# Kernel optimization log

Hardware: AMD Instinct MI355X
Metric: run time of the kernel (lower is better)

## Reference

```python
import jax, jax.numpy as jnp
import numpy as np

N0, N1 = 30000, 20000
N = N0 + N1
E = 400000
H0, H1, H2 = 4, 4, 1
DH = 64            # num_hidden
NC = 16            # num_classes
IN = 128           # per-type input feature dim
SLOPE = 0.2        # leaky relu negative slope


def setup_inputs() -> dict:
    key = jax.random.key(0)
    ks = iter(jax.random.split(key, 48))
    rn = lambda shape, s=0.05: jax.random.normal(next(ks), shape, jnp.float32) * s
    ri = lambda shape: jax.random.randint(next(ks), shape, 0, N, jnp.int32)
    inp = {
        'features0': rn((N0, IN), 1.0),
        'features1': rn((N1, IN), 1.0),
        'fc_w0': rn((IN, DH)), 'fc_b0': jnp.zeros((DH,), jnp.float32),
        'fc_w1': rn((IN, DH)), 'fc_b1': jnp.zeros((DH,), jnp.float32),
        'mix_w': jnp.zeros((2, 3, 2), jnp.float32),  # (n_types, num_layers+1, n_graphs)
        # GATConv params stacked over the 2 relation graphs
        'W0': rn((2, DH, H0 * DH)), 'al0': rn((2, H0, DH), 0.1), 'ar0': rn((2, H0, DH), 0.1), 'b0': jnp.zeros((2, H0 * DH), jnp.float32),
        'W1': rn((2, H0 * DH, H1 * DH)), 'al1': rn((2, H1, DH), 0.1), 'ar1': rn((2, H1, DH), 0.1), 'b1': jnp.zeros((2, H1 * DH), jnp.float32),
        'W2': rn((2, H1 * DH, H2 * NC)), 'al2': rn((2, H2, NC), 0.1), 'ar2': rn((2, H2, NC), 0.1), 'b2': jnp.zeros((2, H2 * NC), jnp.float32),
        'res2': rn((2, H1 * DH, H2 * NC)),  # res_fc for last layer (in != out*heads)
        'src0': ri((E,)), 'dst0': ri((E,)),
        'src1': ri((E,)), 'dst1': ri((E,)),
    }
    return inp


def gat_conv(h, src, dst, W, al, ar, b, H, D, res_mode, res_w, act):
    # h: (N, in)  ->  (N, H, D)
    feat = (h @ W).reshape(N, H, D)
    el = jnp.sum(feat * al, axis=-1)   # (N, H)
    er = jnp.sum(feat * ar, axis=-1)   # (N, H)
    e = jax.nn.leaky_relu(el[src] + er[dst], SLOPE)  # (E, H)
    # edge softmax over incoming edges of each dst node
    m = jax.ops.segment_max(e, dst, num_segments=N)
    ex = jnp.exp(e - m[dst])
    den = jax.ops.segment_sum(ex, dst, num_segments=N)
    alpha = ex / den[dst]                              # (E, H)
    out = jax.ops.segment_sum(feat[src] * alpha[..., None], dst, num_segments=N)
    if res_mode == 'id':
        out = out + h.reshape(N, H, D)
    elif res_mode == 'fc':
        out = out + (h @ res_w).reshape(N, H, D)
    out = out + b.reshape(1, H, D)
    return jax.nn.elu(out) if act else out


def _forward(features0, features1, fc_w0, fc_b0, fc_w1, fc_b1, mix_w,
             W0, al0, ar0, b0, W1, al1, ar1, b1, W2, al2, ar2, b2, res2,
             src0, dst0, src1, dst1):
    nt = jnp.concatenate([jnp.zeros(N0, jnp.int32), jnp.ones(N1, jnp.int32)])
    w = jax.nn.softmax(mix_w, axis=2)  # (types, layers+1, graphs)
    h = jnp.concatenate([features0 @ fc_w0 + fc_b0, features1 @ fc_w1 + fc_b1], axis=0)
    srcs, dsts = (src0, src1), (dst0, dst1)
    layers = [
        (W0, al0, ar0, b0, H0, DH, None, True),
        (W1, al1, ar1, b1, H1, DH, 'id', True),
    ]
    for l, (W, al, ar, b, H, D, rm, act) in enumerate(layers):
        acc = 0.
        for i in range(2):
            o = gat_conv(h, srcs[i], dsts[i], W[i], al[i], ar[i], b[i], H, D, rm, None, act)
            acc = acc + o.reshape(N, H * D) * w[nt, l, i][:, None]
        h = acc
    logits = 0.
    for i in range(2):
        o = gat_conv(h, srcs[i], dsts[i], W2[i], al2[i], ar2[i], b2[i], H2, NC, 'fc', res2[i], False)
        logits = logits + o.mean(axis=1) * w[nt, 2, i][:, None]
    return logits


def reference(features0, features1, fc_w0, fc_b0, fc_w1, fc_b1, mix_w,
              W0, al0, ar0, b0, W1, al1, ar1, b1, W2, al2, ar2, b2, res2,
              src0, dst0, src1, dst1):
    return _forward(features0, features1, fc_w0, fc_b0, fc_w1, fc_b1, mix_w,
                    W0, al0, ar0, b0, W1, al1, ar1, b1, W2, al2, ar2, b2, res2,
                    src0, dst0, src1, dst1)
```

## Files before the change

kernel.cpp:

```cpp
#include <hip/hip_runtime.h>
#include <hip/hip_bf16.h>

#define NN   50000
#define NN0  30000
#define EE   400000
#define NB_SCAN ((NN + 1023) / 1024)
#define NRT   3125
#define NGRP  ((NRT + 3) / 4)
#define NT0   1875

typedef unsigned short u16;
typedef unsigned int   u32;

typedef __attribute__((ext_vector_type(8))) __bf16 bf16x8;
typedef __attribute__((ext_vector_type(4))) float  f32x4;

__device__ __forceinline__ float bf2f(u16 u){ return __uint_as_float(((u32)u)<<16); }
__device__ __forceinline__ float lo16(u32 u){ return __uint_as_float(u<<16); }
__device__ __forceinline__ float hi16(u32 u){ return __uint_as_float(u & 0xffff0000u); }
__device__ __forceinline__ u16 f2bf(float f){
  u32 x = __float_as_uint(f);
  x += 0x7fffu + ((x>>16)&1u);
  return (u16)(x>>16);
}
__device__ __forceinline__ float elu_f(float x){ return x>0.f ? x : __expf(x)-1.f; }
__device__ __forceinline__ float lrelu(float x){ return x>0.f ? x : 0.2f*x; }
__device__ __forceinline__ bf16x8 ld_frag(const u16* p){
  uint4 v = *(const uint4*)p;
  return __builtin_bit_cast(bf16x8, v);
}
__device__ __forceinline__ bf16x8 cvt8(const float* p){
  float4 u = ((const float4*)p)[0];
  float4 v = ((const float4*)p)[1];
  u32 w0 = (u32)f2bf(u.x) | ((u32)f2bf(u.y)<<16);
  u32 w1 = (u32)f2bf(u.z) | ((u32)f2bf(u.w)<<16);
  u32 w2 = (u32)f2bf(v.x) | ((u32)f2bf(v.y)<<16);
  u32 w3 = (u32)f2bf(v.z) | ((u32)f2bf(v.w)<<16);
  uint4 r{w0,w1,w2,w3};
  return __builtin_bit_cast(bf16x8, r);
}

__global__ __launch_bounds__(256) void k_prep(
    const float* __restrict__ mix_w, float* __restrict__ wsoft,
    const float* __restrict__ W0, u16* __restrict__ W0p,
    const float* __restrict__ W1, u16* __restrict__ W1p,
    const float* __restrict__ W2, const float* __restrict__ res2, u16* __restrict__ W2p,
    const float* __restrict__ fcw0, const float* __restrict__ fcw1, u16* __restrict__ Fp,
    const float* __restrict__ al0, const float* __restrict__ ar0, u16* __restrict__ Vp)
{
  int t = blockIdx.x*256 + threadIdx.x;
  if (t < 6){
    float a0 = mix_w[t*2+0], a1 = mix_w[t*2+1];
    float mx = fmaxf(a0,a1);
    float e0 = __expf(a0-mx), e1 = __expf(a1-mx);
    wsoft[t*2+0] = e0/(e0+e1); wsoft[t*2+1] = e1/(e0+e1);
  }
  if (t < 4096){
    int gg = t>>11, fi = t&2047;
    int lane = fi&63, kb = (fi>>6)&1, ct = fi>>7;
    int q = lane>>4, c = lane&15;
    const float* src = W0 + (size_t)gg*16384;
    u16* o = W0p + (size_t)gg*16384 + (size_t)fi*8;
    #pragma unroll
    for (int j=0;j<8;j++) o[j] = f2bf(src[(size_t)(kb*32+q*8+j)*256 + ct*16 + c]);
  } else if (t < 20480){
    int u = t - 4096;
    int gg = u>>13, fi = u&8191;
    int lane = fi&63, kb = (fi>>6)&7, ct = fi>>9;
    int q = lane>>4, c = lane&15;
    const float* src = W1 + (size_t)gg*65536;
    u16* o = W1p + (size_t)gg*65536 + (size_t)fi*8;
    #pragma unroll
    for (int j=0;j<8;j++) o[j] = f2bf(src[(size_t)(kb*32+q*8+j)*256 + ct*16 + c]);
  } else if (t < 22528){
    int fi = t - 20480;
    int lane = fi&63, kb = (fi>>6)&7, ct = fi>>9;
    int q = lane>>4, c = lane&15;
    int cl = ct*16 + c;
    int i = cl>>5, which = (cl>>4)&1;
    const float* src = which ? res2 : W2;
    u16* o = W2p + (size_t)fi*8;
    #pragma unroll
    for (int j=0;j<8;j++) o[j] = f2bf(src[(size_t)i*4096 + (size_t)(kb*32+q*8+j)*16 + (cl&15)]);
  } else if (t < 24576){
    int u = t - 22528;
    int tt = u>>10, fi = u&1023;
    int lane = fi&63, kb = (fi>>6)&3, ct = fi>>8;
    int q = lane>>4, c = lane&15;
    const float* src = tt ? fcw1 : fcw0;
    u16* o = Fp + (size_t)tt*8192 + (size_t)fi*8;
    #pragma unroll
    for (int j=0;j<8;j++) o[j] = f2bf(src[(size_t)(kb*32+q*8+j)*64 + ct*16 + c]);
  } else if (t < 25600){
    int u = t - 24576;
    int fi = u>>3, j = u&7;
    int lane = fi&63, kb = fi>>6;
    int q = lane>>4, c = lane&15;
    int k = kb*32 + q*8 + j;
    int which = c>>3, g=(c>>2)&1, h=c&3;
    const float* sel = (which ? ar0 : al0) + (size_t)(g*4+h)*64;
    const float* Wrow = W0 + (size_t)g*16384 + (size_t)k*256 + h*64;
    float s=0.f;
    #pragma unroll 8
    for (int d=0;d<64;d++) s = fmaf(Wrow[d], sel[d], s);
    Vp[(size_t)fi*8 + j] = f2bf(s);
  }
}

__global__ void k_count2(const int* __restrict__ d0, const int* __restrict__ d1,
                         int* __restrict__ cnt2){
  int t = blockIdx.x*256 + threadIdx.x;
  int g = blockIdx.y;
  if (t < EE) atomicAdd(&cnt2[g*NN + (g ? d1[t] : d0[t])], 1);
}

__global__ __launch_bounds__(1024) void k_scan1(const int* __restrict__ cnt2,
                                                int* __restrict__ row2, int* __restrict__ bsum){
  __shared__ int wsum[16];
  int g = blockIdx.y;
  int lane = threadIdx.x & 63, wid = threadIdx.x >> 6;
  int i = blockIdx.x*1024 + threadIdx.x;
  int v = (i < NN) ? cnt2[g*NN + i] : 0;
  int x = v;
  #pragma unroll
  for (int off = 1; off < 64; off <<= 1){
    int y = __shfl_up(x, off, 64);
    if (lane >= off) x += y;
  }
  if (lane == 63) wsum[wid] = x;
  __syncthreads();
  if (wid == 0 && lane < 16){
    int s = wsum[lane];
    #pragma unroll
    for (int off = 1; off < 16; off <<= 1){
      int y = __shfl_up(s, off, 16);
      if (lane >= off) s += y;
    }
    wsum[lane] = s;
  }
  __syncthreads();
  int incl = x + (wid ? wsum[wid-1] : 0);
  if (i < NN) row2[(size_t)g*(NN+1) + i] = incl - v;
  if (threadIdx.x == 1023) bsum[g*NB_SCAN + blockIdx.x] = incl;
}

__global__ __launch_bounds__(128) void k_scan2(const int* __restrict__ bsum, int* __restrict__ boff){
  int g = threadIdx.x >> 6, lane = threadIdx.x & 63;
  int v = (lane < NB_SCAN) ? bsum[g*NB_SCAN + lane] : 0;
  int x = v;
  #pragma unroll
  for (int off = 1; off < 64; off <<= 1){
    int y = __shfl_up(x, off, 64);
    if (lane >= off) x += y;
  }
  if (lane < NB_SCAN) boff[g*NB_SCAN + lane] = x - v;
}

__global__ __launch_bounds__(1024) void k_scan3(int* __restrict__ row2, const int* __restrict__ boff){
  int g = blockIdx.y;
  int i = blockIdx.x*1024 + threadIdx.x;
  if (i < NN) row2[(size_t)g*(NN+1) + i] += boff[g*NB_SCAN + blockIdx.x];
  if (blockIdx.x == 0 && threadIdx.x == 0) row2[(size_t)g*(NN+1) + NN] = EE;
}

__global__ void k_scatter2(const int* __restrict__ s0, const int* __restrict__ d0,
                           const int* __restrict__ s1, const int* __restrict__ d1,
                           const int* __restrict__ row2, int* __restrict__ fill2,
                           u16* __restrict__ col2, u16* __restrict__ dstOf){
  int t = blockIdx.x*256 + threadIdx.x;
  int g = blockIdx.y;
  if (t >= EE) return;
  int d = g ? d1[t] : d0[t];
  int s = g ? s1[t] : s0[t];
  int pos = atomicAdd(&fill2[g*NN + d], 1);
  size_t slot = (size_t)g*EE + row2[(size_t)g*(NN+1) + d] + pos;
  col2[slot]  = (u16)s;
  dstOf[slot] = (u16)d;
}

__global__ void k_alpha4(const u16* __restrict__ col2, const u16* __restrict__ dstOf,
                         const float* __restrict__ el, const float* __restrict__ er,
                         size_t elStride, float* __restrict__ xbuf){
  int t = blockIdx.x*256 + threadIdx.x;
  int g = blockIdx.y;
  if (t >= EE) return;
  size_t slot = (size_t)g*EE + t;
  int s = col2[slot], d = dstOf[slot];
  const float* elg = el + (size_t)g*elStride;
  const float* erg = er + (size_t)g*elStride;
  float4 e4 = ((const float4*)elg)[s];
  float4 r4 = ((const float4*)erg)[d];
  float4 x;
  x.x = __expf(lrelu(e4.x + r4.x));
  x.y = __expf(lrelu(e4.y + r4.y));
  x.z = __expf(lrelu(e4.z + r4.z));
  x.w = __expf(lrelu(e4.w + r4.w));
  ((float4*)xbuf)[slot] = x;
}

__global__ void k_alpha1(const u16* __restrict__ col2, const u16* __restrict__ dstOf,
                         const float* __restrict__ el2, const float* __restrict__ er2,
                         float* __restrict__ xb2){
  int t = blockIdx.x*256 + threadIdx.x;
  int g = blockIdx.y;
  if (t >= EE) return;
  size_t slot = (size_t)g*EE + t;
  int s = col2[slot], d = dstOf[slot];
  xb2[slot] = __expf(lrelu(el2[(size_t)g*NN + s] + er2[(size_t)g*NN + d]));
}

__global__ __launch_bounds__(256) void k_inproj_m(
    const float* __restrict__ f0, const float* __restrict__ f1,
    const u16* __restrict__ Fp, const float* __restrict__ fb0, const float* __restrict__ fb1,
    u16* __restrict__ h0)
{
  int wv = threadIdx.x>>6, ln = threadIdx.x&63;
  int ti = blockIdx.x*4 + wv;
  if (ti >= NRT) return;
  int q = ln>>4, c = ln&15;
  int type = (ti < NT0) ? 0 : 1;
  const float* F = type ? f1 : f0;
  int rbase = type ? (ti*16 - NN0) : ti*16;
  const u16* Bg = Fp + (size_t)type*8192;
  const float* bb = type ? fb1 : fb0;
  f32x4 acc[4] = {};
  const float* Ap = F + (size_t)(rbase + c)*128;
  #pragma unroll
  for (int kb=0; kb<4; kb++){
    bf16x8 a = cvt8(Ap + kb*32 + q*8);
    #pragma unroll
    for (int ct=0; ct<4; ct++){
      bf16x8 b = ld_frag(Bg + ((size_t)(ct*4+kb)*64 + ln)*8);
      acc[ct] = __builtin_amdgcn_mfma_f32_16x16x32_bf16(a, b, acc[ct], 0,0,0);
    }
  }
  #pragma unroll
  for (int ct=0; ct<4; ct++){
    float bv = bb[ct*16+c];
    #pragma unroll
    for (int j=0;j<4;j++){
      int row = ti*16 + q*4 + j;
      h0[(size_t)row*64 + ct*16 + c] = f2bf(acc[ct][j] + bv);
    }
  }
}

__global__ __launch_bounds__(256) void k_eler0(
    const u16* __restrict__ h0, const u16* __restrict__ Vp,
    float* __restrict__ elA, float* __restrict__ erA)
{
  int wv = threadIdx.x>>6, ln = threadIdx.x&63;
  int ti = blockIdx.x*4 + wv;
  if (ti >= NRT) return;
  int q = ln>>4, c = ln&15;
  f32x4 acc = {};
  const u16* Ap = h0 + (size_t)(ti*16 + c)*64 + q*8;
  #pragma unroll
  for (int kb=0; kb<2; kb++){
    bf16x8 a = ld_frag(Ap + kb*32);
    bf16x8 b = ld_frag(Vp + ((size_t)(kb*64 + ln))*8);
    acc = __builtin_amdgcn_mfma_f32_16x16x32_bf16(a, b, acc, 0,0,0);
  }
  int which = c>>3, g = (c>>2)&1, h = c&3;
  float* dst = (which ? erA : elA) + (size_t)g*NN*4;
  #pragma unroll
  for (int j=0;j<4;j++){
    int row = ti*16 + q*4 + j;
    dst[row*4 + h] = acc[j];
  }
}

__global__ __launch_bounds__(256) void k_agg0(
    const int* __restrict__ row2, const u16* __restrict__ col2,
    const float* __restrict__ xbuf, const u16* __restrict__ h0,
    u16* __restrict__ aggB, size_t aggStride)
{
  int wv = threadIdx.x>>6, ln = threadIdx.x&63;
  int n = blockIdx.x*4 + wv;
  #pragma unroll
  for (int g=0; g<2; g++){
    const int* rw = row2 + (size_t)g*(NN+1);
    const u16* cl = col2 + (size_t)g*EE;
    const float4* xb = (const float4*)xbuf + (size_t)g*EE;
    int beg = rw[n], end = rw[n+1];
    float d0=0.f,d1=0.f,d2=0.f,d3=0.f;
    float a0=0.f,a1=0.f,a2=0.f,a3=0.f;
    int k = beg;
    for (; k+2<=end; k+=2){
      int s0 = cl[k], s1 = cl[k+1];
      float4 x0 = xb[k], x1 = xb[k+1];
      float v0 = bf2f(h0[(size_t)s0*64 + ln]);
      float v1 = bf2f(h0[(size_t)s1*64 + ln]);
      d0 += x0.x+x1.x; d1 += x0.y+x1.y; d2 += x0.z+x1.z; d3 += x0.w+x1.w;
      a0 += x0.x*v0 + x1.x*v1; a1 += x0.y*v0 + x1.y*v1;
      a2 += x0.z*v0 + x1.z*v1; a3 += x0.w*v0 + x1.w*v1;
    }
    for (; k<end; k++){
      int s = cl[k];
      float4 x = xb[k];
      float v = bf2f(h0[(size_t)s*64 + ln]);
      d0+=x.x; d1+=x.y; d2+=x.z; d3+=x.w;
      a0+=x.x*v; a1+=x.y*v; a2+=x.z*v; a3+=x.w*v;
    }
    bool has = (end > beg);
    a0 = has ? a0/d0 : 0.f; a1 = has ? a1/d1 : 0.f;
    a2 = has ? a2/d2 : 0.f; a3 = has ? a3/d3 : 0.f;
    u16* og = aggB + (size_t)g*aggStride + (size_t)n*256 + ln;
    og[0]   = f2bf(a0); og[64]  = f2bf(a1);
    og[128] = f2bf(a2); og[192] = f2bf(a3);
  }
}

__global__ __launch_bounds__(256) void k_head0(
    const u16* __restrict__ aggB, size_t aggStride,
    const u16* __restrict__ W0p, const float* __restrict__ b0,
    const float* __restrict__ wsoft, u16* __restrict__ h1)
{
  int wv = threadIdx.x>>6, ln = threadIdx.x&63;
  int ti = blockIdx.x*4 + wv;
  if (ti >= NRT) return;
  int q = ln>>4, c = ln&15;
  int type = (ti < NT0) ? 0 : 1;
  float wg0 = wsoft[type*6 + 0];
  float wg1 = wsoft[type*6 + 1];
  for (int h=0; h<4; h++){
    f32x4 acc[2][4] = {};
    #pragma unroll
    for (int g=0; g<2; g++){
      const u16* Ap = aggB + (size_t)g*aggStride + (size_t)(ti*16 + c)*256 + h*64 + q*8;
      const u16* Bg = W0p + (size_t)g*16384;
      #pragma unroll
      for (int kb=0; kb<2; kb++){
        bf16x8 a = ld_frag(Ap + kb*32);
        #pragma unroll
        for (int ct=0; ct<4; ct++){
          int ctg = h*4 + ct;
          bf16x8 b = ld_frag(Bg + ((size_t)(ctg*2 + kb)*64 + ln)*8);
          acc[g][ct] = __builtin_amdgcn_mfma_f32_16x16x32_bf16(a, b, acc[g][ct], 0,0,0);
        }
      }
    }
    #pragma unroll
    for (int ct=0; ct<4; ct++){
      int colg = h*64 + ct*16 + c;
      float bb0 = b0[colg], bb1 = b0[256 + colg];
      #pragma unroll
      for (int j=0;j<4;j++){
        int row = ti*16 + q*4 + j;
        float o = wg0*elu_f(acc[0][ct][j] + bb0) + wg1*elu_f(acc[1][ct][j] + bb1);
        h1[(size_t)row*256 + colg] = f2bf(o);
      }
    }
  }
}

template<int K>
__global__ __launch_bounds__(256) void k_gemm4(
    const u16* __restrict__ A,
    const u16* __restrict__ Bp, size_t bpStride,
    const float* __restrict__ al, const float* __restrict__ ar, int alStride,
    u16* __restrict__ feat, size_t featStride,
    float* __restrict__ el, float* __restrict__ er, size_t elStride)
{
  constexpr int KB = K/32;
  int wv = threadIdx.x>>6, ln = threadIdx.x&63;
  int bid = blockIdx.x;
  int g = bid / NGRP, grp = bid % NGRP;
  int split = wv, q = ln>>4, c = ln&15;
  const u16* Bpg = Bp + (size_t)g*bpStride;
  const float* alg = al + (size_t)g*alStride;
  const float* arg = ar + (size_t)g*alStride;
  u16* featg = feat + (size_t)g*featStride;
  float* elg = el + (size_t)g*elStride;
  float* erg = er + (size_t)g*elStride;

  f32x4 acc[4][4] = {};
  int  tbase = grp*4;
  bool valid[4];
  const u16* Ap[4];
  #pragma unroll
  for (int rt=0; rt<4; rt++){
    int ti = tbase + rt;
    valid[rt] = (ti < NRT);
    if (!valid[rt]) ti = NRT-1;
    Ap[rt] = A + (size_t)(ti*16 + c)*K + q*8;
  }
  const u16* Bbase = Bpg + ((size_t)(split*4)*KB*64 + ln)*8;

  #pragma unroll 2
  for (int kb=0; kb<KB; kb++){
    bf16x8 b[4], a[4];
    #pragma unroll
    for (int ct=0; ct<4; ct++) b[ct] = ld_frag(Bbase + (size_t)(ct*KB + kb)*64*8);
    #pragma unroll
    for (int rt=0; rt<4; rt++) a[rt] = ld_frag(Ap[rt] + kb*32);
    #pragma unroll
    for (int rt=0; rt<4; rt++)
      #pragma unroll
      for (int ct=0; ct<4; ct++)
        acc[rt][ct] = __builtin_amdgcn_mfma_f32_16x16x32_bf16(a[rt], b[ct], acc[rt][ct], 0,0,0);
  }

  float alv[4], arv[4];
  #pragma unroll
  for (int ct=0;ct<4;ct++){
    int cg = (split*4+ct)*16 + c;
    alv[ct] = alg[cg]; arv[ct] = arg[cg];
  }
  #pragma unroll
  for (int rt=0; rt<4; rt++){
    if (!valid[rt]) continue;
    int row0 = (tbase+rt)*16;
    #pragma unroll
    for (int j=0;j<4;j++){
      float ep=0.f, rp=0.f;
      #pragma unroll
      for (int ct=0;ct<4;ct++){ ep += acc[rt][ct][j]*alv[ct]; rp += acc[rt][ct][j]*arv[ct]; }
      #pragma unroll
      for (int off=8; off; off>>=1){ ep += __shfl_xor(ep,off,16); rp += __shfl_xor(rp,off,16); }
      int row = row0 + q*4 + j;
      if (c==0){ elg[row*4+split]=ep; erg[row*4+split]=rp; }
      #pragma unroll
      for (int ct=0;ct<4;ct++)
        featg[(size_t)row*256 + (split*4+ct)*16 + c] = f2bf(acc[rt][ct][j]);
    }
  }
}

template<int RES>
__global__ __launch_bounds__(256) void k_aggNF(
    const int* __restrict__ row2, const u16* __restrict__ col2,
    const float* __restrict__ xbuf,
    const u16* __restrict__ feat, size_t featStride,
    const u16* __restrict__ hres, const float* __restrict__ bias,
    const float* __restrict__ wsoft, int l,
    u16* __restrict__ hout)
{
  int wv = threadIdx.x>>6, ln = threadIdx.x&63;
  int n = blockIdx.x*4 + wv;
  int h = ln>>4;
  int type = (n<NN0)?0:1;
  float rx=0.f, ry=0.f, rz=0.f, rw_=0.f;
  if (RES){
    uint2 r = ((const uint2*)hres)[(size_t)n*64 + ln];
    rx=lo16(r.x); ry=hi16(r.x); rz=lo16(r.y); rw_=hi16(r.y);
  }
  float o0=0.f,o1=0.f,o2=0.f,o3=0.f;
  #pragma unroll
  for (int g=0; g<2; g++){
    const int* rw = row2 + (size_t)g*(NN+1);
    const u16* cl = col2 + (size_t)g*EE;
    const float* xb = xbuf + (size_t)g*EE*4;
    const uint2* fp = (const uint2*)(feat + (size_t)g*featStride);
    int beg = rw[n], end = rw[n+1];
    float den = 0.f;
    float a0=0.f,a1=0.f,a2=0.f,a3=0.f;
    int k = beg;
    for (; k+4<=end; k+=4){
      int s0=cl[k], s1=cl[k+1], s2=cl[k+2], s3=cl[k+3];
      float x0 = xb[(size_t)k*4 + h];
      float x1 = xb[(size_t)(k+1)*4 + h];
      float x2 = xb[(size_t)(k+2)*4 + h];
      float x3 = xb[(size_t)(k+3)*4 + h];
      uint2 f0 = fp[(size_t)s0*64 + ln];
      uint2 f1 = fp[(size_t)s1*64 + ln];
      uint2 f2 = fp[(size_t)s2*64 + ln];
      uint2 f3 = fp[(size_t)s3*64 + ln];
      den += (x0+x1) + (x2+x3);
      a0 += x0*lo16(f0.x) + x1*lo16(f1.x) + x2*lo16(f2.x) + x3*lo16(f3.x);
      a1 += x0*hi16(f0.x) + x1*hi16(f1.x) + x2*hi16(f2.x) + x3*hi16(f3.x);
      a2 += x0*lo16(f0.y) + x1*lo16(f1.y) + x2*lo16(f2.y) + x3*lo16(f3.y);
      a3 += x0*hi16(f0.y) + x1*hi16(f1.y) + x2*hi16(f2.y) + x3*hi16(f3.y);
    }
    for (; k<end; k++){
      int s = cl[k];
      float x = xb[(size_t)k*4 + h];
      uint2 f = fp[(size_t)s*64 + ln];
      den += x;
      a0 += x*lo16(f.x); a1 += x*hi16(f.x); a2 += x*lo16(f.y); a3 += x*hi16(f.y);
    }
    float inv = (end>beg) ? 1.0f/den : 0.f;
    float4 bv = ((const float4*)(bias + g*256))[ln];
    a0 = a0*inv + bv.x; a1 = a1*inv + bv.y; a2 = a2*inv + bv.z; a3 = a3*inv + bv.w;
    if (RES){ a0 += rx; a1 += ry; a2 += rz; a3 += rw_; }
    float w = wsoft[type*6 + l*2 + g];
    o0 += w*elu_f(a0); o1 += w*elu_f(a1); o2 += w*elu_f(a2); o3 += w*elu_f(a3);
  }
  uint2 o;
  o.x = (u32)f2bf(o0) | ((u32)f2bf(o1)<<16);
  o.y = (u32)f2bf(o2) | ((u32)f2bf(o3)<<16);
  ((uint2*)hout)[(size_t)n*64 + ln] = o;
}

__global__ __launch_bounds__(256) void k_gemm2(
    const u16* __restrict__ A, const u16* __restrict__ Bp,
    const float* __restrict__ al2, const float* __restrict__ ar2,
    float* __restrict__ feat16, float* __restrict__ resb,
    float* __restrict__ el2, float* __restrict__ er2)
{
  int wv = threadIdx.x>>6, ln = threadIdx.x&63;
  int wt = blockIdx.x*4 + wv;
  if (wt >= NRT) return;
  int row0 = wt*16;
  int q = ln>>4, c = ln&15;
  f32x4 acc[4] = {};
  const u16* Ap = A + (size_t)(row0 + c)*256 + q*8;
  #pragma unroll
  for (int kb=0; kb<8; kb++){
    bf16x8 a = ld_frag(Ap + kb*32);
    #pragma unroll
    for (int t=0;t<4;t++){
      bf16x8 b = ld_frag(Bp + ((size_t)(t*8 + kb)*64 + ln)*8);
      acc[t] = __builtin_amdgcn_mfma_f32_16x16x32_bf16(a, b, acc[t], 0,0,0);
    }
  }
  #pragma unroll
  for (int i=0;i<2;i++){
    float alv = al2[i*16+c], arv = ar2[i*16+c];
    #pragma unroll
    for (int j=0;j<4;j++){
      float ep = acc[2*i][j]*alv, rp = acc[2*i][j]*arv;
      #pragma unroll
      for (int off=8; off; off>>=1){ ep += __shfl_xor(ep,off,16); rp += __shfl_xor(rp,off,16); }
      if (c==0){
        int row = row0 + q*4 + j;
        el2[(size_t)i*NN + row] = ep; er2[(size_t)i*NN + row] = rp;
      }
    }
    #pragma unroll
    for (int j=0;j<4;j++){
      int row = row0 + q*4 + j;
      feat16[(size_t)i*NN*16 + (size_t)row*16 + c] = acc[2*i][j];
      resb  [(size_t)i*NN*16 + (size_t)row*16 + c] = acc[2*i+1][j];
    }
  }
}

__global__ __launch_bounds__(256) void k_agg2D(
    const int* __restrict__ row2, const u16* __restrict__ col2,
    const float* __restrict__ xb2,
    const float* __restrict__ feat16, const float* __restrict__ resb,
    const float* __restrict__ b2, const float* __restrict__ wsoft,
    float* __restrict__ out)
{
  int t = threadIdx.x;
  int nl = t>>4, j = t&15;
  int n = blockIdx.x*16 + nl;
  int type = (n<NN0)?0:1;
  float o = 0.f;
  #pragma unroll
  for (int i=0;i<2;i++){
    const int* rw = row2 + (size_t)i*(NN+1);
    const u16* cl = col2 + (size_t)i*EE;
    const float* xb = xb2 + (size_t)i*EE;
    const float* f  = feat16 + (size_t)i*NN*16;
    int beg = rw[n], end = rw[n+1];
    float den = 0.f, acc = 0.f;
    int k = beg;
    for (; k+4<=end; k+=4){
      int s0=cl[k], s1=cl[k+1], s2=cl[k+2], s3=cl[k+3];
      float x0 = xb[k], x1 = xb[k+1], x2 = xb[k+2], x3 = xb[k+3];
      float v0 = f[(size_t)s0*16 + j];
      float v1 = f[(size_t)s1*16 + j];
      float v2 = f[(size_t)s2*16 + j];
      float v3 = f[(size_t)s3*16 + j];
      den += (x0+x1) + (x2+x3);
      acc += x0*v0 + x1*v1 + x2*v2 + x3*v3;
    }
    for (; k<end; k++){
      int s = cl[k];
      float x = xb[k];
      den += x;
      acc = fmaf(x, f[(size_t)s*16 + j], acc);
    }
    float inv = (end>beg) ? 1.0f/den : 0.f;
    float oi = acc*inv + b2[i*16+j] + resb[(size_t)i*NN*16 + (size_t)n*16 + j];
    o += oi * wsoft[type*6 + 4 + i];
  }
  out[(size_t)n*16 + j] = o;
}

extern "C" void kernel_launch(void* const* d_in, const int* in_sizes, int n_in,
                              void* d_out, int out_size, void* d_ws, size_t ws_size,
                              hipStream_t stream)
{
  const float* features0 = (const float*)d_in[0];
  const float* features1 = (const float*)d_in[1];
  const float* fc_w0 = (const float*)d_in[2];
  const float* fc_b0 = (const float*)d_in[3];
  const float* fc_w1 = (const float*)d_in[4];
  const float* fc_b1 = (const float*)d_in[5];
  const float* mix_w = (const float*)d_in[6];
  const float* W0  = (const float*)d_in[7];
  const float* al0 = (const float*)d_in[8];
  const float* ar0 = (const float*)d_in[9];
  const float* b0  = (const float*)d_in[10];
  const float* W1  = (const float*)d_in[11];
  const float* al1 = (const float*)d_in[12];
  const float* ar1 = (const float*)d_in[13];
  const float* b1  = (const float*)d_in[14];
  const float* W2  = (const float*)d_in[15];
  const float* al2 = (const float*)d_in[16];
  const float* ar2 = (const float*)d_in[17];
  const float* b2  = (const float*)d_in[18];
  const float* res2= (const float*)d_in[19];
  const int* src[2] = {(const int*)d_in[20], (const int*)d_in[22]};
  const int* dst[2] = {(const int*)d_in[21], (const int*)d_in[23]};
  (void)in_sizes; (void)n_in; (void)out_size; (void)ws_size;

  char* ws = (char*)d_ws;
  size_t off = 0;
  auto alloc = [&](size_t bytes)->char*{
    char* p = ws + off; off += (bytes + 255) & ~(size_t)255; return p;
  };
  float* wsoft = (float*)alloc(64*4);
  u16*   W0p   = (u16*)  alloc((size_t)2*64*256*2);
  u16*   W1p   = (u16*)  alloc((size_t)2*256*256*2);
  u16*   W2p   = (u16*)  alloc((size_t)256*64*2);
  u16*   Fp    = (u16*)  alloc((size_t)2*128*64*2);
  u16*   Vp    = (u16*)  alloc((size_t)64*16*2);
  int*   row2  = (int*)  alloc((size_t)2*(NN+1)*4);
  u16*   col2  = (u16*)  alloc((size_t)2*EE*2);
  u16*   dstOf = (u16*)  alloc((size_t)2*EE*2);
  int*   zeros = (int*)  alloc((size_t)4*NN*4);
  int*   cnt2  = zeros;
  int*   fill2 = zeros + 2*NN;
  int*   bsum  = (int*)alloc((size_t)2*NB_SCAN*4);
  int*   boff  = (int*)alloc((size_t)2*NB_SCAN*4);
  u16*   h0    = (u16*)alloc((size_t)NN*64*2);
  u16*   h1    = (u16*)alloc((size_t)NN*256*2);
  u16*   h2    = (u16*)alloc((size_t)NN*256*2);
  float* elA   = (float*)alloc((size_t)2*NN*4*4);
  float* erA   = (float*)alloc((size_t)2*NN*4*4);
  float* xbuf  = (float*)alloc((size_t)2*EE*4*4);
  size_t featStride = (size_t)NN*256;
  size_t off_D = off;
  u16* regionD = (u16*)alloc(2*featStride*2);
  u16* aggB  = regionD;
  u16* featD = regionD;
  float* feat16 = (float*)(ws + off_D);
  float* resb   = feat16 + (size_t)2*NN*16;
  float* el2    = resb   + (size_t)2*NN*16;
  float* er2    = el2    + (size_t)2*NN;

  k_prep<<<100,256,0,stream>>>(mix_w, wsoft, W0, W0p, W1, W1p, W2, res2, W2p,
                               fc_w0, fc_w1, Fp, al0, ar0, Vp);

  hipMemsetAsync(zeros, 0, (size_t)4*NN*4, stream);
  {
    dim3 gE((EE+255)/256, 2), gS(NB_SCAN, 2);
    k_count2 <<<gE,256,0,stream>>>(dst[0], dst[1], cnt2);
    k_scan1  <<<gS,1024,0,stream>>>(cnt2, row2, bsum);
    k_scan2  <<<1,128,0,stream>>>(bsum, boff);
    k_scan3  <<<gS,1024,0,stream>>>(row2, boff);
    k_scatter2<<<gE,256,0,stream>>>(src[0], dst[0], src[1], dst[1], row2, fill2, col2, dstOf);
  }

  k_inproj_m<<<NGRP,256,0,stream>>>(features0, features1, Fp, fc_b0, fc_b1, h0);
  k_eler0   <<<NGRP,256,0,stream>>>(h0, Vp, elA, erA);

  dim3 gE((EE+255)/256, 2);

  k_alpha4<<<gE,256,0,stream>>>(col2, dstOf, elA, erA, (size_t)NN*4, xbuf);
  k_agg0 <<<NN/4,256,0,stream>>>(row2, col2, xbuf, h0, aggB, featStride);
  k_head0<<<NGRP,256,0,stream>>>(aggB, featStride, W0p, b0, wsoft, h1);

  k_gemm4<256><<<2*NGRP,256,0,stream>>>(h1, W1p, (size_t)256*256, al1, ar1, 256,
                                        featD, featStride, elA, erA, (size_t)NN*4);
  k_alpha4<<<gE,256,0,stream>>>(col2, dstOf, elA, erA, (size_t)NN*4, xbuf);
  k_aggNF<1><<<NN/4,256,0,stream>>>(row2, col2, xbuf, featD, featStride,
                                    h1, b1, wsoft, 1, h2);

  k_gemm2<<<NGRP,256,0,stream>>>(h2, W2p, al2, ar2, feat16, resb, el2, er2);
  k_alpha1<<<gE,256,0,stream>>>(col2, dstOf, el2, er2, xbuf);
  k_agg2D<<<NN/16,256,0,stream>>>(row2, col2, xbuf, feat16, resb, b2, wsoft, (float*)d_out);
}
```

Measured before the change: 459.5 us.

## Compute softmax denominators per node, fuse layer-0 aggregation with head GEMM

Drops the per-edge dstOf array. Edge exp-scores are now computed per destination node over the CSR row, which also yields an inverse softmax denominator per node, so the aggregation kernels no longer sum denominators. Layer-0 aggregation and the head GEMM are fused through an LDS tile, which removes the aggB round trip through global memory. An 8-wide unrolled gather loop is added to the layer-1 aggregation. The catch is that the per-node alpha kernels use one thread per node, so degree imbalance and uncoalesced xbuf writes may hurt.

```diff
diff --git a/kernel.cpp b/kernel.cpp
--- a/kernel.cpp
+++ b/kernel.cpp
@@ -166,47 +166,67 @@
 __global__ void k_scatter2(const int* __restrict__ s0, const int* __restrict__ d0,
                            const int* __restrict__ s1, const int* __restrict__ d1,
                            const int* __restrict__ row2, int* __restrict__ fill2,
-                           u16* __restrict__ col2, u16* __restrict__ dstOf){
+                           u16* __restrict__ col2){
   int t = blockIdx.x*256 + threadIdx.x;
   int g = blockIdx.y;
   if (t >= EE) return;
   int d = g ? d1[t] : d0[t];
   int s = g ? s1[t] : s0[t];
   int pos = atomicAdd(&fill2[g*NN + d], 1);
-  size_t slot = (size_t)g*EE + row2[(size_t)g*(NN+1) + d] + pos;
-  col2[slot]  = (u16)s;
-  dstOf[slot] = (u16)d;
-}
-
-__global__ void k_alpha4(const u16* __restrict__ col2, const u16* __restrict__ dstOf,
-                         const float* __restrict__ el, const float* __restrict__ er,
-                         size_t elStride, float* __restrict__ xbuf){
-  int t = blockIdx.x*256 + threadIdx.x;
+  col2[(size_t)g*EE + row2[(size_t)g*(NN+1) + d] + pos] = (u16)s;
+}
+
+__global__ void k_alphaden4(const int* __restrict__ row2, const u16* __restrict__ col2,
+                            const float* __restrict__ el, const float* __restrict__ er,
+                            size_t elStride, float* __restrict__ xbuf,
+                            float* __restrict__ invd){
+  int n = blockIdx.x*256 + threadIdx.x;
   int g = blockIdx.y;
-  if (t >= EE) return;
-  size_t slot = (size_t)g*EE + t;
-  int s = col2[slot], d = dstOf[slot];
+  if (n >= NN) return;
+  const int* rw = row2 + (size_t)g*(NN+1);
+  const u16* cl = col2 + (size_t)g*EE;
   const float* elg = el + (size_t)g*elStride;
-  const float* erg = er + (size_t)g*elStride;
-  float4 e4 = ((const float4*)elg)[s];
-  float4 r4 = ((const float4*)erg)[d];
-  float4 x;
-  x.x = __expf(lrelu(e4.x + r4.x));
-  x.y = __expf(lrelu(e4.y + r4.y));
-  x.z = __expf(lrelu(e4.z + r4.z));
-  x.w = __expf(lrelu(e4.w + r4.w));
-  ((float4*)xbuf)[slot] = x;
-}
-
-__global__ void k_alpha1(const u16* __restrict__ col2, const u16* __restrict__ dstOf,
-                         const float* __restrict__ el2, const float* __restrict__ er2,
-                         float* __restrict__ xb2){
-  int t = blockIdx.x*256 + threadIdx.x;
+  float4 r4 = ((const float4*)(er + (size_t)g*elStride))[n];
+  float4* xb = (float4*)xbuf + (size_t)g*EE;
+  int beg = rw[n], end = rw[n+1];
+  float d0=0.f,d1=0.f,d2=0.f,d3=0.f;
+  for (int k=beg; k<end; k++){
+    int s = cl[k];
+    float4 e = ((const float4*)elg)[s];
+    float4 x;
+    x.x = __expf(lrelu(e.x + r4.x));
+    x.y = __expf(lrelu(e.y + r4.y));
+    x.z = __expf(lrelu(e.z + r4.z));
+    x.w = __expf(lrelu(e.w + r4.w));
+    xb[k] = x;
+    d0 += x.x; d1 += x.y; d2 += x.z; d3 += x.w;
+  }
+  bool has = (end > beg);
+  float4 iv;
+  iv.x = has ? 1.f/d0 : 0.f; iv.y = has ? 1.f/d1 : 0.f;
+  iv.z = has ? 1.f/d2 : 0.f; iv.w = has ? 1.f/d3 : 0.f;
+  ((float4*)invd)[(size_t)g*NN + n] = iv;
+}
+
+__global__ void k_alphaden1(const int* __restrict__ row2, const u16* __restrict__ col2,
+                            const float* __restrict__ el2, const float* __restrict__ er2,
+                            float* __restrict__ xb2, float* __restrict__ invd1){
+  int n = blockIdx.x*256 + threadIdx.x;
   int g = blockIdx.y;
-  if (t >= EE) return;
-  size_t slot = (size_t)g*EE + t;
-  int s = col2[slot], d = dstOf[slot];
-  xb2[slot] = __expf(lrelu(el2[(size_t)g*NN + s] + er2[(size_t)g*NN + d]));
+  if (n >= NN) return;
+  const int* rw = row2 + (size_t)g*(NN+1);
+  const u16* cl = col2 + (size_t)g*EE;
+  const float* elg = el2 + (size_t)g*NN;
+  float ern = er2[(size_t)g*NN + n];
+  float* xb = xb2 + (size_t)g*EE;
+  int beg = rw[n], end = rw[n+1];
+  float d = 0.f;
+  for (int k=beg; k<end; k++){
+    float x = __expf(lrelu(elg[cl[k]] + ern));
+    xb[k] = x;
+    d += x;
+  }
+  invd1[(size_t)g*NN + n] = (end>beg) ? 1.f/d : 0.f;
 }
 
 __global__ __launch_bounds__(256) void k_inproj_m(
@@ -270,86 +290,79 @@
   }
 }
 
-__global__ __launch_bounds__(256) void k_agg0(
+__global__ __launch_bounds__(256) void k_fused0(
     const int* __restrict__ row2, const u16* __restrict__ col2,
-    const float* __restrict__ xbuf, const u16* __restrict__ h0,
-    u16* __restrict__ aggB, size_t aggStride)
-{
-  int wv = threadIdx.x>>6, ln = threadIdx.x&63;
-  int n = blockIdx.x*4 + wv;
-  #pragma unroll
-  for (int g=0; g<2; g++){
-    const int* rw = row2 + (size_t)g*(NN+1);
-    const u16* cl = col2 + (size_t)g*EE;
-    const float4* xb = (const float4*)xbuf + (size_t)g*EE;
-    int beg = rw[n], end = rw[n+1];
-    float d0=0.f,d1=0.f,d2=0.f,d3=0.f;
-    float a0=0.f,a1=0.f,a2=0.f,a3=0.f;
-    int k = beg;
-    for (; k+2<=end; k+=2){
-      int s0 = cl[k], s1 = cl[k+1];
-      float4 x0 = xb[k], x1 = xb[k+1];
-      float v0 = bf2f(h0[(size_t)s0*64 + ln]);
-      float v1 = bf2f(h0[(size_t)s1*64 + ln]);
-      d0 += x0.x+x1.x; d1 += x0.y+x1.y; d2 += x0.z+x1.z; d3 += x0.w+x1.w;
-      a0 += x0.x*v0 + x1.x*v1; a1 += x0.y*v0 + x1.y*v1;
-      a2 += x0.z*v0 + x1.z*v1; a3 += x0.w*v0 + x1.w*v1;
-    }
-    for (; k<end; k++){
-      int s = cl[k];
-      float4 x = xb[k];
-      float v = bf2f(h0[(size_t)s*64 + ln]);
-      d0+=x.x; d1+=x.y; d2+=x.z; d3+=x.w;
-      a0+=x.x*v; a1+=x.y*v; a2+=x.z*v; a3+=x.w*v;
-    }
-    bool has = (end > beg);
-    a0 = has ? a0/d0 : 0.f; a1 = has ? a1/d1 : 0.f;
-    a2 = has ? a2/d2 : 0.f; a3 = has ? a3/d3 : 0.f;
-    u16* og = aggB + (size_t)g*aggStride + (size_t)n*256 + ln;
-    og[0]   = f2bf(a0); og[64]  = f2bf(a1);
-    og[128] = f2bf(a2); og[192] = f2bf(a3);
-  }
-}
-
-__global__ __launch_bounds__(256) void k_head0(
-    const u16* __restrict__ aggB, size_t aggStride,
+    const float* __restrict__ xbuf, const float* __restrict__ invd,
+    const u16* __restrict__ h0,
     const u16* __restrict__ W0p, const float* __restrict__ b0,
     const float* __restrict__ wsoft, u16* __restrict__ h1)
 {
+  __shared__ u16 hs[2][16][264];
   int wv = threadIdx.x>>6, ln = threadIdx.x&63;
-  int ti = blockIdx.x*4 + wv;
-  if (ti >= NRT) return;
+  int ti = blockIdx.x;
+  #pragma unroll
+  for (int r=0; r<4; r++){
+    int nl = wv*4 + r;
+    int n = ti*16 + nl;
+    #pragma unroll
+    for (int g=0; g<2; g++){
+      const int* rw = row2 + (size_t)g*(NN+1);
+      const u16* cl = col2 + (size_t)g*EE;
+      const float4* xb = (const float4*)xbuf + (size_t)g*EE;
+      int beg = rw[n], end = rw[n+1];
+      float a0=0.f,a1=0.f,a2=0.f,a3=0.f;
+      int k = beg;
+      for (; k+2<=end; k+=2){
+        int s0 = cl[k], s1 = cl[k+1];
+        float4 x0 = xb[k], x1 = xb[k+1];
+        float v0 = bf2f(h0[(size_t)s0*64 + ln]);
+        float v1 = bf2f(h0[(size_t)s1*64 + ln]);
+        a0 += x0.x*v0 + x1.x*v1; a1 += x0.y*v0 + x1.y*v1;
+        a2 += x0.z*v0 + x1.z*v1; a3 += x0.w*v0 + x1.w*v1;
+      }
+      for (; k<end; k++){
+        int s = cl[k];
+        float4 x = xb[k];
+        float v = bf2f(h0[(size_t)s*64 + ln]);
+        a0+=x.x*v; a1+=x.y*v; a2+=x.z*v; a3+=x.w*v;
+      }
+      float4 iv = ((const float4*)invd)[(size_t)g*NN + n];
+      hs[g][nl][0*64+ln] = f2bf(a0*iv.x);
+      hs[g][nl][1*64+ln] = f2bf(a1*iv.y);
+      hs[g][nl][2*64+ln] = f2bf(a2*iv.z);
+      hs[g][nl][3*64+ln] = f2bf(a3*iv.w);
+    }
+  }
+  __syncthreads();
   int q = ln>>4, c = ln&15;
+  int h = wv;
   int type = (ti < NT0) ? 0 : 1;
   float wg0 = wsoft[type*6 + 0];
   float wg1 = wsoft[type*6 + 1];
-  for (int h=0; h<4; h++){
-    f32x4 acc[2][4] = {};
-    #pragma unroll
-    for (int g=0; g<2; g++){
-      const u16* Ap = aggB + (size_t)g*aggStride + (size_t)(ti*16 + c)*256 + h*64 + q*8;
-      const u16* Bg = W0p + (size_t)g*16384;
-      #pragma unroll
-      for (int kb=0; kb<2; kb++){
-        bf16x8 a = ld_frag(Ap + kb*32);
-        #pragma unroll
-        for (int ct=0; ct<4; ct++){
-          int ctg = h*4 + ct;
-          bf16x8 b = ld_frag(Bg + ((size_t)(ctg*2 + kb)*64 + ln)*8);
-          acc[g][ct] = __builtin_amdgcn_mfma_f32_16x16x32_bf16(a, b, acc[g][ct], 0,0,0);
-        }
+  f32x4 acc[2][4] = {};
+  #pragma unroll
+  for (int g=0; g<2; g++){
+    const u16* Bg = W0p + (size_t)g*16384;
+    #pragma unroll
+    for (int kb=0; kb<2; kb++){
+      bf16x8 a = ld_frag(&hs[g][c][h*64 + kb*32 + q*8]);
+      #pragma unroll
+      for (int ct=0; ct<4; ct++){
+        int ctg = h*4 + ct;
+        bf16x8 b = ld_frag(Bg + ((size_t)(ctg*2 + kb)*64 + ln)*8);
+        acc[g][ct] = __builtin_amdgcn_mfma_f32_16x16x32_bf16(a, b, acc[g][ct], 0,0,0);
       }
     }
-    #pragma unroll
-    for (int ct=0; ct<4; ct++){
-      int colg = h*64 + ct*16 + c;
-      float bb0 = b0[colg], bb1 = b0[256 + colg];
-      #pragma unroll
-      for (int j=0;j<4;j++){
-        int row = ti*16 + q*4 + j;
-        float o = wg0*elu_f(acc[0][ct][j] + bb0) + wg1*elu_f(acc[1][ct][j] + bb1);
-        h1[(size_t)row*256 + colg] = f2bf(o);
-      }
+  }
+  #pragma unroll
+  for (int ct=0; ct<4; ct++){
+    int colg = h*64 + ct*16 + c;
+    float bb0 = b0[colg], bb1 = b0[256 + colg];
+    #pragma unroll
+    for (int j=0;j<4;j++){
+      int row = ti*16 + q*4 + j;
+      float o = wg0*elu_f(acc[0][ct][j] + bb0) + wg1*elu_f(acc[1][ct][j] + bb1);
+      h1[(size_t)row*256 + colg] = f2bf(o);
     }
   }
 }
@@ -430,7 +443,7 @@
 template<int RES>
 __global__ __launch_bounds__(256) void k_aggNF(
     const int* __restrict__ row2, const u16* __restrict__ col2,
-    const float* __restrict__ xbuf,
+    const float* __restrict__ xbuf, const float* __restrict__ invd,
     const u16* __restrict__ feat, size_t featStride,
     const u16* __restrict__ hres, const float* __restrict__ bias,
     const float* __restrict__ wsoft, int l,
@@ -453,9 +466,22 @@
     const float* xb = xbuf + (size_t)g*EE*4;
     const uint2* fp = (const uint2*)(feat + (size_t)g*featStride);
     int beg = rw[n], end = rw[n+1];
-    float den = 0.f;
     float a0=0.f,a1=0.f,a2=0.f,a3=0.f;
     int k = beg;
+    for (; k+8<=end; k+=8){
+      int s[8]; float x[8]; uint2 f[8];
+      #pragma unroll
+      for (int u=0; u<8; u++) s[u] = cl[k+u];
+      #pragma unroll
+      for (int u=0; u<8; u++) x[u] = xb[(size_t)(k+u)*4 + h];
+      #pragma unroll
+      for (int u=0; u<8; u++) f[u] = fp[(size_t)s[u]*64 + ln];
+      #pragma unroll
+      for (int u=0; u<8; u++){
+        a0 += x[u]*lo16(f[u].x); a1 += x[u]*hi16(f[u].x);
+        a2 += x[u]*lo16(f[u].y); a3 += x[u]*hi16(f[u].y);
+      }
+    }
     for (; k+4<=end; k+=4){
       int s0=cl[k], s1=cl[k+1], s2=cl[k+2], s3=cl[k+3];
       float x0 = xb[(size_t)k*4 + h];
@@ -466,7 +492,6 @@
       uint2 f1 = fp[(size_t)s1*64 + ln];
       uint2 f2 = fp[(size_t)s2*64 + ln];
       uint2 f3 = fp[(size_t)s3*64 + ln];
-      den += (x0+x1) + (x2+x3);
       a0 += x0*lo16(f0.x) + x1*lo16(f1.x) + x2*lo16(f2.x) + x3*lo16(f3.x);
       a1 += x0*hi16(f0.x) + x1*hi16(f1.x) + x2*hi16(f2.x) + x3*hi16(f3.x);
       a2 += x0*lo16(f0.y) + x1*lo16(f1.y) + x2*lo16(f2.y) + x3*lo16(f3.y);
@@ -476,10 +501,9 @@
       int s = cl[k];
       float x = xb[(size_t)k*4 + h];
       uint2 f = fp[(size_t)s*64 + ln];
-      den += x;
       a0 += x*lo16(f.x); a1 += x*hi16(f.x); a2 += x*lo16(f.y); a3 += x*hi16(f.y);
     }
-    float inv = (end>beg) ? 1.0f/den : 0.f;
+    float inv = invd[((size_t)g*NN + n)*4 + h];
     float4 bv = ((const float4*)(bias + g*256))[ln];
     a0 = a0*inv + bv.x; a1 = a1*inv + bv.y; a2 = a2*inv + bv.z; a3 = a3*inv + bv.w;
     if (RES){ a0 += rx; a1 += ry; a2 += rz; a3 += rw_; }
@@ -538,7 +562,7 @@
 
 __global__ __launch_bounds__(256) void k_agg2D(
     const int* __restrict__ row2, const u16* __restrict__ col2,
-    const float* __restrict__ xb2,
+    const float* __restrict__ xb2, const float* __restrict__ invd1,
     const float* __restrict__ feat16, const float* __restrict__ resb,
     const float* __restrict__ b2, const float* __restrict__ wsoft,
     float* __restrict__ out)
@@ -555,7 +579,7 @@
     const float* xb = xb2 + (size_t)i*EE;
     const float* f  = feat16 + (size_t)i*NN*16;
     int beg = rw[n], end = rw[n+1];
-    float den = 0.f, acc = 0.f;
+    float acc = 0.f;
     int k = beg;
     for (; k+4<=end; k+=4){
       int s0=cl[k], s1=cl[k+1], s2=cl[k+2], s3=cl[k+3];
@@ -564,16 +588,12 @@
       float v1 = f[(size_t)s1*16 + j];
       float v2 = f[(size_t)s2*16 + j];
       float v3 = f[(size_t)s3*16 + j];
-      den += (x0+x1) + (x2+x3);
       acc += x0*v0 + x1*v1 + x2*v2 + x3*v3;
     }
     for (; k<end; k++){
-      int s = cl[k];
-      float x = xb[k];
-      den += x;
-      acc = fmaf(x, f[(size_t)s*16 + j], acc);
-    }
-    float inv = (end>beg) ? 1.0f/den : 0.f;
+      acc = fmaf(xb[k], f[(size_t)cl[k]*16 + j], acc);
+    }
+    float inv = invd1[(size_t)i*NN + n];
     float oi = acc*inv + b2[i*16+j] + resb[(size_t)i*NN*16 + (size_t)n*16 + j];
     o += oi * wsoft[type*6 + 4 + i];
   }
@@ -621,7 +641,6 @@
   u16*   Vp    = (u16*)  alloc((size_t)64*16*2);
   int*   row2  = (int*)  alloc((size_t)2*(NN+1)*4);
   u16*   col2  = (u16*)  alloc((size_t)2*EE*2);
-  u16*   dstOf = (u16*)  alloc((size_t)2*EE*2);
   int*   zeros = (int*)  alloc((size_t)4*NN*4);
   int*   cnt2  = zeros;
   int*   fill2 = zeros + 2*NN;
@@ -632,12 +651,12 @@
   u16*   h2    = (u16*)alloc((size_t)NN*256*2);
   float* elA   = (float*)alloc((size_t)2*NN*4*4);
   float* erA   = (float*)alloc((size_t)2*NN*4*4);
+  float* invd  = (float*)alloc((size_t)2*NN*4*4);
+  float* invd1 = (float*)alloc((size_t)2*NN*4);
   float* xbuf  = (float*)alloc((size_t)2*EE*4*4);
   size_t featStride = (size_t)NN*256;
   size_t off_D = off;
-  u16* regionD = (u16*)alloc(2*featStride*2);
-  u16* aggB  = regionD;
-  u16* featD = regionD;
+  u16* featD = (u16*)alloc(2*featStride*2);
   float* feat16 = (float*)(ws + off_D);
   float* resb   = feat16 + (size_t)2*NN*16;
   float* el2    = resb   + (size_t)2*NN*16;
@@ -653,25 +672,24 @@
     k_scan1  <<<gS,1024,0,stream>>>(cnt2, row2, bsum);
     k_scan2  <<<1,128,0,stream>>>(bsum, boff);
     k_scan3  <<<gS,1024,0,stream>>>(row2, boff);
-    k_scatter2<<<gE,256,0,stream>>>(src[0], dst[0], src[1], dst[1], row2, fill2, col2, dstOf);
+    k_scatter2<<<gE,256,0,stream>>>(src[0], dst[0], src[1], dst[1], row2, fill2, col2);
   }
 
   k_inproj_m<<<NGRP,256,0,stream>>>(features0, features1, Fp, fc_b0, fc_b1, h0);
   k_eler0   <<<NGRP,256,0,stream>>>(h0, Vp, elA, erA);
 
-  dim3 gE((EE+255)/256, 2);
-
-  k_alpha4<<<gE,256,0,stream>>>(col2, dstOf, elA, erA, (size_t)NN*4, xbuf);
-  k_agg0 <<<NN/4,256,0,stream>>>(row2, col2, xbuf, h0, aggB, featStride);
-  k_head0<<<NGRP,256,0,stream>>>(aggB, featStride, W0p, b0, wsoft, h1);
+  dim3 gN((NN+255)/256, 2);
+
+  k_alphaden4<<<gN,256,0,stream>>>(row2, col2, elA, erA, (size_t)NN*4, xbuf, invd);
+  k_fused0<<<NRT,256,0,stream>>>(row2, col2, xbuf, invd, h0, W0p, b0, wsoft, h1);
 
   k_gemm4<256><<<2*NGRP,256,0,stream>>>(h1, W1p, (size_t)256*256, al1, ar1, 256,
                                         featD, featStride, elA, erA, (size_t)NN*4);
-  k_alpha4<<<gE,256,0,stream>>>(col2, dstOf, elA, erA, (size_t)NN*4, xbuf);
-  k_aggNF<1><<<NN/4,256,0,stream>>>(row2, col2, xbuf, featD, featStride,
+  k_alphaden4<<<gN,256,0,stream>>>(row2, col2, elA, erA, (size_t)NN*4, xbuf, invd);
+  k_aggNF<1><<<NN/4,256,0,stream>>>(row2, col2, xbuf, invd, featD, featStride,
                                     h1, b1, wsoft, 1, h2);
 
   k_gemm2<<<NGRP,256,0,stream>>>(h2, W2p, al2, ar2, feat16, resb, el2, er2);
-  k_alpha1<<<gE,256,0,stream>>>(col2, dstOf, el2, er2, xbuf);
-  k_agg2D<<<NN/16,256,0,stream>>>(row2, col2, xbuf, feat16, resb, b2, wsoft, (float*)d_out);
-}
+  k_alphaden1<<<gN,256,0,stream>>>(row2, col2, el2, er2, xbuf, invd1);
+  k_agg2D<<<NN/16,256,0,stream>>>(row2, col2, xbuf, invd1, feat16, resb, b2, wsoft, (float*)d_out);
+}
```

New measurement: 488.3 us. +6.3%, slower.
